# Optimization experiments

Measured on AMD Instinct MI355X. Metric: run time of the kernel, lower is better.

Reference implementation:

```python
import jax, jax.numpy as jnp
import numpy as np

VOCAB = 32000
D = 256          # d_model == hidden_size
L = 2            # num_layers
B, S = 16, 512


def ste_quant_int4(w):
    """Int4 fake-quant with straight-through estimator.
    scale = max|w|/7 (clamped), q = round(w/scale).clip(-8,7)*scale;
    gradient passes through unchanged (identity)."""
    scale = jnp.maximum(jnp.max(jnp.abs(w)) / 7.0, 1e-8)
    q = jnp.round(w / scale).clip(-8.0, 7.0) * scale
    return w + jax.lax.stop_gradient(q - w)


def setup_inputs() -> dict:
    key = jax.random.key(0)
    ks = jax.random.split(key, 8)
    x = jax.random.randint(ks[0], (B, S), 0, VOCAB, dtype=jnp.int32)
    emb_w = jax.random.normal(ks[1], (VOCAB, D), dtype=jnp.float32) * 0.02
    # kaiming-uniform-ish init for linear weights
    lim_ih = 1.0 / np.sqrt(D)
    w_ih = jax.random.uniform(ks[2], (L, 4 * D, D), jnp.float32, -lim_ih, lim_ih)
    w_hh = jax.random.uniform(ks[3], (L, 4 * D, D), jnp.float32, -lim_ih, lim_ih)
    b_ih = jnp.zeros((L, 4 * D), jnp.float32)
    b_hh = jnp.zeros((L, 4 * D), jnp.float32)
    lim_fc = 1.0 / np.sqrt(D)
    fc_w = jax.random.uniform(ks[4], (VOCAB, D), jnp.float32, -lim_fc, lim_fc)
    fc_b = jnp.zeros((VOCAB,), jnp.float32)
    return {"x": x, "emb_w": emb_w, "w_ih": w_ih, "b_ih": b_ih,
            "w_hh": w_hh, "b_hh": b_hh, "fc_w": fc_w, "fc_b": fc_b}


def reference(x, emb_w, w_ih, b_ih, w_hh, b_hh, fc_w, fc_b):
    # quantize each weight once (per-tensor scale, per layer for stacked weights)
    emb_q = ste_quant_int4(emb_w)
    wih_q = jax.vmap(ste_quant_int4)(w_ih)   # [L, 4D, D]
    whh_q = jax.vmap(ste_quant_int4)(w_hh)   # [L, 4D, D]
    fcw_q = ste_quant_int4(fc_w)

    emb = emb_q[x]                            # [B, S, D]
    nlayers = w_ih.shape[0]
    h0 = jnp.zeros((nlayers, x.shape[0], D), emb.dtype)
    c0 = jnp.zeros_like(h0)

    def step(carry, xt):                      # xt: [B, D]
        hs, cs = carry
        h = xt
        new_h, new_c = [], []
        for l in range(nlayers):
            gates = (h @ wih_q[l].T + b_ih[l]
                     + hs[l] @ whh_q[l].T + b_hh[l])   # [B, 4D]
            i, f, g, o = jnp.split(gates, 4, axis=-1)
            i = jax.nn.sigmoid(i)
            f = jax.nn.sigmoid(f)
            g = jnp.tanh(g)
            o = jax.nn.sigmoid(o)
            c = f * cs[l] + i * g
            h = o * jnp.tanh(c)
            new_h.append(h)
            new_c.append(c)
        return (jnp.stack(new_h), jnp.stack(new_c)), h

    (_, _), outs = jax.lax.scan(step, (h0, c0), emb.transpose(1, 0, 2))
    out = outs.transpose(1, 0, 2)             # [B, S, D]
    logits = out @ fcw_q.T + fc_b             # [B, S, VOCAB]
    return logits
```

## Files before the change

### kernel.cpp

```cpp
#include <hip/hip_runtime.h>
#include <hip/hip_bf16.h>
#include <stdint.h>

typedef __attribute__((ext_vector_type(8))) short bf16x8;
typedef __attribute__((ext_vector_type(4))) float f32x4;

#define NB   16
#define SEQ  512
#define DM   256
#define G4   1024
#define VOC  32000
#define TOK  (NB*SEQ)

#define OF_SC     0
#define OF_AMAX   64
#define OF_FLAG   128
#define OF_KEMB   16384
#define OF_KWIH0  (OF_KEMB  + TOK*DM*2)
#define OF_KFC    (OF_KWIH0 + G4*DM*2)
#define OF_WL0    (OF_KFC   + VOC*DM*2)
#define OF_WFF    (OF_WL0   + 512*64*16)
#define OF_WL1    (OF_WFF   + 512*64*16)
#define OF_HX0    (OF_WL1   + 512*64*16)
#define OF_HX1    (OF_HX0   + 4*16384)
#define OF_XG     (OF_HX1   + 4*16384)
#define OF_HOUT   (OF_XG    + (size_t)TOK*G4*4)

__device__ __forceinline__ unsigned short bf16b(float f) {
  __hip_bfloat16 h = __float2bfloat16(f);
  return *reinterpret_cast<unsigned short*>(&h);
}
__device__ __forceinline__ float bf16f(short u) {
  return __uint_as_float(((unsigned)(unsigned short)u) << 16);
}
__device__ __forceinline__ float quant_k_val(float w, float s) {
  float k = rintf(w / s);
  return fminf(fmaxf(k, -8.f), 7.f);
}
__device__ __forceinline__ float sigf(float x) { return 1.f / (1.f + expf(-x)); }

__device__ __forceinline__ void gload_lds16(const void* g, void* l) {
  __builtin_amdgcn_global_load_lds(
      (const __attribute__((address_space(1))) void*)g,
      (__attribute__((address_space(3))) void*)l, 16, 0, 0);
}

__device__ __forceinline__ bf16x8 ld_frag_sys(const void* p) {
  bf16x8 r;
  asm volatile("global_load_dwordx4 %0, %1, off sc0 sc1" : "=v"(r) : "v"(p));
  return r;
}
__device__ __forceinline__ void st_frag_sys(void* p, bf16x8 v) {
  asm volatile("global_store_dwordx4 %0, %1, off sc0 sc1" :: "v"(p), "v"(v) : "memory");
}
__device__ __forceinline__ void vm_drain() {
  asm volatile("s_waitcnt vmcnt(0)" ::: "memory");
  __builtin_amdgcn_sched_barrier(0);
}

__device__ __forceinline__ void spin_ge(int* p, int tgt) {
  int it = 0;
  while (__hip_atomic_load(p, __ATOMIC_RELAXED, __HIP_MEMORY_SCOPE_AGENT) < tgt) {
    __builtin_amdgcn_s_sleep(1);
    if (++it > (1 << 15)) break;
  }
}
__device__ __forceinline__ void flag_set(int* p, int v) {
  __hip_atomic_store(p, v, __ATOMIC_RELAXED, __HIP_MEMORY_SCOPE_AGENT);
}

__global__ void k_init(unsigned int* amax, int* flags) {
  if (threadIdx.x < 8) amax[threadIdx.x] = 0u;
  flags[threadIdx.x] = 0;
}

__global__ void k_absmax(const float* __restrict__ p, int n, unsigned int* amax) {
  float m = 0.f;
  for (int i = blockIdx.x * blockDim.x + threadIdx.x; i < n; i += gridDim.x * blockDim.x)
    m = fmaxf(m, fabsf(p[i]));
  #pragma unroll
  for (int off = 32; off > 0; off >>= 1)
    m = fmaxf(m, __shfl_down(m, off));
  if ((threadIdx.x & 63) == 0) atomicMax(amax, __float_as_uint(m));
}

__global__ void k_finalize(const unsigned int* __restrict__ amax, float* __restrict__ sc) {
  int i = threadIdx.x;
  if (i < 6)       sc[i] = fmaxf(__uint_as_float(amax[i]) / 7.0f, 1e-8f);
  else if (i == 6) sc[i] = 1.0f;
}

__global__ void k_quant_kbf16(const float* __restrict__ src, ushort* __restrict__ dst,
                              int n4, const float* __restrict__ sc, int slot) {
  int i = blockIdx.x * blockDim.x + threadIdx.x;
  if (i >= n4) return;
  const float s = sc[slot];
  float4 w = ((const float4*)src)[i];
  ushort4 o;
  o.x = bf16b(quant_k_val(w.x, s));
  o.y = bf16b(quant_k_val(w.y, s));
  o.z = bf16b(quant_k_val(w.z, s));
  o.w = bf16b(quant_k_val(w.w, s));
  ((ushort4*)dst)[i] = o;
}

__global__ void k_gather(const int* __restrict__ x, const float* __restrict__ emb,
                         const float* __restrict__ sc, ushort* __restrict__ out) {
  int i = blockIdx.x * blockDim.x + threadIdx.x;
  if (i >= TOK * 64) return;
  int tok = i >> 6, d4 = i & 63;
  const float s = sc[0];
  int row = x[tok];
  float4 w = *(const float4*)(emb + (size_t)row * DM + d4 * 4);
  ushort4 o;
  o.x = bf16b(quant_k_val(w.x, s));
  o.y = bf16b(quant_k_val(w.y, s));
  o.z = bf16b(quant_k_val(w.z, s));
  o.w = bf16b(quant_k_val(w.w, s));
  ((ushort4*)out)[i] = o;
}

__global__ void k_packrec(const float* __restrict__ src, bf16x8* __restrict__ dst,
                          const float* __restrict__ sc, int slot, int mode) {
  int q = blockIdx.x * blockDim.x + threadIdx.x;
  if (q >= 512 * 64) return;
  int l = q & 63, kf = (q >> 6) & 7, i = (q >> 9) & 1, w = (q >> 10) & 3, g = (q >> 12) & 7;
  int row = mode ? (g * 128 + (w * 2 + i) * 16 + (l & 15))
                 : (w * 256 + g * 32 + i * 16 + (l & 15));
  int kb = kf * 32 + ((l >> 4) & 3) * 8;
  const float s = sc[slot];
  const float* p = src + (size_t)row * DM + kb;
  bf16x8 o;
  #pragma unroll
  for (int e = 0; e < 8; ++e) o[e] = (short)bf16b(quant_k_val(p[e], s));
  dst[q] = o;
}

__global__ __launch_bounds__(256) void k_gemm(
    const ushort* __restrict__ A, const ushort* __restrict__ B,
    float* __restrict__ C, int M, int N,
    const float* __restrict__ s1, const float* __restrict__ s2,
    const float* __restrict__ bias1, const float* __restrict__ bias2)
{
  __shared__ alignas(16) ushort As[128 * 64];
  __shared__ alignas(16) ushort Bs[128 * 64];
  const int tid  = threadIdx.x;
  const int lane = tid & 63;
  const int wid  = tid >> 6;
  const size_t m0 = (size_t)blockIdx.x * 128;
  const size_t n0 = (size_t)blockIdx.y * 128;
  const int wm = (wid >> 1) * 64;
  const int wn = (wid & 1) * 64;
  const int r  = tid >> 3;
  const int c8 = (tid & 7) * 8;

  f32x4 acc[4][4];
  #pragma unroll
  for (int m = 0; m < 4; ++m)
    #pragma unroll
    for (int n = 0; n < 4; ++n) acc[m][n] = (f32x4){0.f, 0.f, 0.f, 0.f};

  for (int k0 = 0; k0 < DM; k0 += 64) {
    #pragma unroll
    for (int i = 0; i < 4; ++i) {
      gload_lds16(A + (m0 + i * 32 + r) * DM + k0 + c8, (char*)As + i * 4096 + wid * 1024);
      gload_lds16(B + (n0 + i * 32 + r) * DM + k0 + c8, (char*)Bs + i * 4096 + wid * 1024);
    }
    __syncthreads();
    #pragma unroll
    for (int kk = 0; kk < 2; ++kk) {
      const int ko = (kk * 32 + ((lane >> 4) << 3)) * 2;
      bf16x8 af[4], bfr[4];
      #pragma unroll
      for (int m = 0; m < 4; ++m)
        af[m] = *(const bf16x8*)((const char*)As + (wm + m * 16 + (lane & 15)) * 128 + ko);
      #pragma unroll
      for (int n = 0; n < 4; ++n)
        bfr[n] = *(const bf16x8*)((const char*)Bs + (wn + n * 16 + (lane & 15)) * 128 + ko);
      #pragma unroll
      for (int m = 0; m < 4; ++m)
        #pragma unroll
        for (int n = 0; n < 4; ++n)
          acc[m][n] = __builtin_amdgcn_mfma_f32_16x16x32_bf16(af[m], bfr[n], acc[m][n], 0, 0, 0);
    }
    __syncthreads();
  }

  const float alpha = s1[0] * s2[0];
  const int cl = lane & 15;
  const int rq = (lane >> 4) * 4;
  #pragma unroll
  for (int n = 0; n < 4; ++n) {
    const size_t col = n0 + wn + n * 16 + cl;
    float badd = 0.f;
    if (bias1) badd += bias1[col];
    if (bias2) badd += bias2[col];
    #pragma unroll
    for (int m = 0; m < 4; ++m) {
      const size_t rowb = m0 + wm + m * 16 + rq;
      #pragma unroll
      for (int q = 0; q < 4; ++q)
        C[(rowb + q) * (size_t)N + col] = acc[m][n][q] * alpha + badd;
    }
  }
}

__global__ __launch_bounds__(512) void k_rec4(
    const bf16x8* __restrict__ WL0, const bf16x8* __restrict__ WFF,
    const bf16x8* __restrict__ WL1, const float* __restrict__ XG,
    ushort* __restrict__ HX0, ushort* __restrict__ HX1,
    ushort* __restrict__ HOUT, int* __restrict__ flags,
    const float* __restrict__ sc,
    const float* __restrict__ bih, const float* __restrict__ bhh)
{
  if (blockIdx.x & 7) return;
  const int m = blockIdx.x >> 3;
  if (m >= 16) return;
  const int role = m >> 3, g = m & 7;
  const int tid = threadIdx.x, lane = tid & 63, w = tid >> 6;
  const int kg = lane >> 4, cb = lane & 15;
  const int r0 = tid & 31, b = tid >> 5;
  const int gw = (g * 4 + (w >> 1)) * 2 + (w & 1);
  __shared__ float Gl[4 * 32 * 17];
  __shared__ alignas(16) ushort hp[1024];
  int* F0 = flags;
  int* F1 = flags + 8 * 32;
  const int fl = ((r0 >> 3) << 4) | b;

  if (role == 0) {
    bf16x8 a[8];
    #pragma unroll
    for (int c = 0; c < 8; ++c) a[c] = WL0[((gw * 8 + c) << 6) + lane];
    const float s2 = sc[2];
    float cc = 0.f;
    for (int t = 0; t < SEQ; ++t) {
      const size_t xb = ((size_t)(b * 512 + t) << 10) + g * 32 + r0;
      float xv0 = XG[xb], xv1 = XG[xb + 256], xv2 = XG[xb + 512], xv3 = XG[xb + 768];
      if (tid < 16) spin_ge((tid < 8) ? F0 + tid * 32 : F1 + (tid - 8) * 32,
                            (tid < 8) ? t : t - 3);
      __syncthreads();
      f32x4 acc = {0.f, 0.f, 0.f, 0.f};
      if (t > 0) {
        const char* hb = (const char*)HX0 + (size_t)((t - 1) & 3) * 16384 + lane * 16;
        bf16x8 bp[16];
        #pragma unroll
        for (int c = 0; c < 8; ++c) {
          bp[2 * c]     = ld_frag_sys(hb + c * 2048);
          bp[2 * c + 1] = ld_frag_sys(hb + c * 2048 + 1024);
        }
        vm_drain();
        #pragma unroll
        for (int c = 0; c < 8; ++c) {
          acc = __builtin_amdgcn_mfma_f32_16x16x32_bf16(a[c], bp[2 * c],     acc, 0, 0, 0);
          acc = __builtin_amdgcn_mfma_f32_16x16x32_bf16(a[c], bp[2 * c + 1], acc, 0, 0, 0);
        }
      }
      #pragma unroll
      for (int q = 0; q < 4; ++q)
        Gl[((w >> 1) * 32 + (w & 1) * 16 + kg * 4 + q) * 17 + cb] = acc[q];
      __syncthreads();
      {
        float g0 = xv0 + s2 * Gl[(0 * 32 + r0) * 17 + b];
        float g1 = xv1 + s2 * Gl[(1 * 32 + r0) * 17 + b];
        float g2 = xv2 + s2 * Gl[(2 * 32 + r0) * 17 + b];
        float g3 = xv3 + s2 * Gl[(3 * 32 + r0) * 17 + b];
        float i_ = sigf(g0), f_ = sigf(g1), gg = tanhf(g2), o_ = sigf(g3);
        cc = f_ * cc + i_ * gg;
        float h = o_ * tanhf(cc);
        unsigned short p1 = bf16b(h);
        float r1 = h - bf16f((short)p1);
        unsigned short p2 = bf16b(r1);
        hp[fl * 8 + (r0 & 7)]       = p1;
        hp[512 + fl * 8 + (r0 & 7)] = p2;
      }
      __syncthreads();
      if (tid < 128)
        st_frag_sys(HX0 + (size_t)(t & 3) * 8192 + g * 1024 + tid * 8,
                    *(const bf16x8*)(hp + tid * 8));
      vm_drain();
      __syncthreads();
      if (tid == 0) flag_set(F0 + g * 32, t + 1);
    }
  } else {
    bf16x8 aI[8], aH[8];
    #pragma unroll
    for (int c = 0; c < 8; ++c) {
      aI[c] = WFF[((gw * 8 + c) << 6) + lane];
      aH[c] = WL1[((gw * 8 + c) << 6) + lane];
    }
    const float s3 = sc[3], s4 = sc[4];
    const int jb = G4 + g * 32 + r0;
    const float bb0 = bih[jb]       + bhh[jb];
    const float bb1 = bih[jb + 256] + bhh[jb + 256];
    const float bb2 = bih[jb + 512] + bhh[jb + 512];
    const float bb3 = bih[jb + 768] + bhh[jb + 768];
    float cc = 0.f;
    for (int t = 0; t < SEQ; ++t) {
      if (tid < 8) spin_ge(F1 + tid * 32, t);
      __syncthreads();
      f32x4 accH = {0.f, 0.f, 0.f, 0.f};
      if (t > 0) {
        const char* hb = (const char*)HX1 + (size_t)((t - 1) & 3) * 16384 + lane * 16;
        bf16x8 bp[16];
        #pragma unroll
        for (int c = 0; c < 8; ++c) {
          bp[2 * c]     = ld_frag_sys(hb + c * 2048);
          bp[2 * c + 1] = ld_frag_sys(hb + c * 2048 + 1024);
        }
        vm_drain();
        #pragma unroll
        for (int c = 0; c < 8; ++c) {
          accH = __builtin_amdgcn_mfma_f32_16x16x32_bf16(aH[c], bp[2 * c],     accH, 0, 0, 0);
          accH = __builtin_amdgcn_mfma_f32_16x16x32_bf16(aH[c], bp[2 * c + 1], accH, 0, 0, 0);
        }
      }
      if (tid < 8) spin_ge(F0 + tid * 32, t + 1);
      __syncthreads();
      f32x4 accI = {0.f, 0.f, 0.f, 0.f};
      {
        const char* hb = (const char*)HX0 + (size_t)(t & 3) * 16384 + lane * 16;
        bf16x8 bp[16];
        #pragma unroll
        for (int c = 0; c < 8; ++c) {
          bp[2 * c]     = ld_frag_sys(hb + c * 2048);
          bp[2 * c + 1] = ld_frag_sys(hb + c * 2048 + 1024);
        }
        vm_drain();
        #pragma unroll
        for (int c = 0; c < 8; ++c) {
          accI = __builtin_amdgcn_mfma_f32_16x16x32_bf16(aI[c], bp[2 * c],     accI, 0, 0, 0);
          accI = __builtin_amdgcn_mfma_f32_16x16x32_bf16(aI[c], bp[2 * c + 1], accI, 0, 0, 0);
        }
      }
      #pragma unroll
      for (int q = 0; q < 4; ++q)
        Gl[((w >> 1) * 32 + (w & 1) * 16 + kg * 4 + q) * 17 + cb] = s3 * accI[q] + s4 * accH[q];
      __syncthreads();
      {
        float g0 = bb0 + Gl[(0 * 32 + r0) * 17 + b];
        float g1 = bb1 + Gl[(1 * 32 + r0) * 17 + b];
        float g2 = bb2 + Gl[(2 * 32 + r0) * 17 + b];
        float g3 = bb3 + Gl[(3 * 32 + r0) * 17 + b];
        float i_ = sigf(g0), f_ = sigf(g1), gg = tanhf(g2), o_ = sigf(g3);
        cc = f_ * cc + i_ * gg;
        float h = o_ * tanhf(cc);
        unsigned short p1 = bf16b(h);
        float r1 = h - bf16f((short)p1);
        unsigned short p2 = bf16b(r1);
        HOUT[((size_t)b * 512 + t) * 256 + g * 32 + r0] = p1;
        hp[fl * 8 + (r0 & 7)]       = p1;
        hp[512 + fl * 8 + (r0 & 7)] = p2;
      }
      __syncthreads();
      if (tid < 128)
        st_frag_sys(HX1 + (size_t)(t & 3) * 8192 + g * 1024 + tid * 8,
                    *(const bf16x8*)(hp + tid * 8));
      vm_drain();
      __syncthreads();
      if (tid == 0) flag_set(F1 + g * 32, t + 1);
    }
  }
}

extern "C" void kernel_launch(void* const* d_in, const int* in_sizes, int n_in,
                              void* d_out, int out_size, void* d_ws, size_t ws_size,
                              hipStream_t stream) {
  const int*   x   = (const int*)d_in[0];
  const float* emb = (const float*)d_in[1];
  const float* wih = (const float*)d_in[2];
  const float* bih = (const float*)d_in[3];
  const float* whh = (const float*)d_in[4];
  const float* bhh = (const float*)d_in[5];
  const float* fcw = (const float*)d_in[6];
  const float* fcb = (const float*)d_in[7];
  float* out = (float*)d_out;

  char* ws = (char*)d_ws;
  float*        SC    = (float*)(ws + OF_SC);
  unsigned int* AMAX  = (unsigned int*)(ws + OF_AMAX);
  int*          FLAGS = (int*)(ws + OF_FLAG);
  ushort*       KEMB  = (ushort*)(ws + OF_KEMB);
  ushort*       KWIH0 = (ushort*)(ws + OF_KWIH0);
  ushort*       KFC   = (ushort*)(ws + OF_KFC);
  bf16x8*       WL0   = (bf16x8*)(ws + OF_WL0);
  bf16x8*       WFF   = (bf16x8*)(ws + OF_WFF);
  bf16x8*       WL1   = (bf16x8*)(ws + OF_WL1);
  ushort*       HX0   = (ushort*)(ws + OF_HX0);
  ushort*       HX1   = (ushort*)(ws + OF_HX1);
  float*        XG    = (float*)(ws + OF_XG);
  ushort*       HOUT  = (ushort*)(ws + OF_HOUT);

  const int nw = G4 * DM;

  k_init<<<1, 1024, 0, stream>>>(AMAX, FLAGS);
  k_absmax<<<2048, 256, 0, stream>>>(emb,      VOC * DM, AMAX + 0);
  k_absmax<<<256,  256, 0, stream>>>(wih,      nw,       AMAX + 1);
  k_absmax<<<256,  256, 0, stream>>>(whh,      nw,       AMAX + 2);
  k_absmax<<<256,  256, 0, stream>>>(wih + nw, nw,       AMAX + 3);
  k_absmax<<<256,  256, 0, stream>>>(whh + nw, nw,       AMAX + 4);
  k_absmax<<<2048, 256, 0, stream>>>(fcw,      VOC * DM, AMAX + 5);
  k_finalize<<<1, 8, 0, stream>>>(AMAX, SC);

  k_gather<<<TOK * 64 / 256, 256, 0, stream>>>(x, emb, SC, KEMB);
  k_quant_kbf16<<<nw / 4 / 256,       256, 0, stream>>>(wih, KWIH0, nw / 4,       SC, 1);
  k_quant_kbf16<<<VOC * DM / 4 / 256, 256, 0, stream>>>(fcw, KFC,   VOC * DM / 4, SC, 5);
  k_packrec<<<128, 256, 0, stream>>>(whh,      WL0, SC, 2, 0);
  k_packrec<<<128, 256, 0, stream>>>(wih + nw, WFF, SC, 3, 0);
  k_packrec<<<128, 256, 0, stream>>>(whh + nw, WL1, SC, 4, 0);

  dim3 g1(TOK / 128, G4 / 128);
  k_gemm<<<g1, 256, 0, stream>>>(KEMB, KWIH0, XG, TOK, G4, SC + 0, SC + 1, bih, bhh);

  k_rec4<<<128, 512, 0, stream>>>(WL0, WFF, WL1, XG, HX0, HX1, HOUT,
                                  FLAGS, SC, bih, bhh);

  dim3 g2(TOK / 128, VOC / 128);
  k_gemm<<<g2, 256, 0, stream>>>(HOUT, KFC, out, TOK, VOC, SC + 5, SC + 6, fcb, nullptr);
}
```

Before: 2.784 ms.

## Use per-step hidden-state buffers to drop backpressure waits and batch layer-1 loads

Measured after the change: 2.714 ms. 1.03x faster.

```diff
diff --git a/kernel.cpp b/kernel.cpp
--- a/kernel.cpp
+++ b/kernel.cpp
@@ -22,8 +22,8 @@
 #define OF_WFF    (OF_WL0   + 512*64*16)
 #define OF_WL1    (OF_WFF   + 512*64*16)
 #define OF_HX0    (OF_WL1   + 512*64*16)
-#define OF_HX1    (OF_HX0   + 4*16384)
-#define OF_XG     (OF_HX1   + 4*16384)
+#define OF_HX1    (OF_HX0   + (size_t)SEQ*16384)
+#define OF_XG     (OF_HX1   + (size_t)SEQ*16384)
 #define OF_HOUT   (OF_XG    + (size_t)TOK*G4*4)
 
 __device__ __forceinline__ unsigned short bf16b(float f) {
@@ -45,9 +45,9 @@
       (__attribute__((address_space(3))) void*)l, 16, 0, 0);
 }
 
-__device__ __forceinline__ bf16x8 ld_frag_sys(const void* p) {
+__device__ __forceinline__ bf16x8 ld_frag_c(const void* p) {
   bf16x8 r;
-  asm volatile("global_load_dwordx4 %0, %1, off sc0 sc1" : "=v"(r) : "v"(p));
+  asm volatile("global_load_dwordx4 %0, %1, off sc0" : "=v"(r) : "v"(p));
   return r;
 }
 __device__ __forceinline__ void st_frag_sys(void* p, bf16x8 v) {
@@ -55,6 +55,10 @@
 }
 __device__ __forceinline__ void vm_drain() {
   asm volatile("s_waitcnt vmcnt(0)" ::: "memory");
+  __builtin_amdgcn_sched_barrier(0);
+}
+__device__ __forceinline__ void vm_wait16() {
+  asm volatile("s_waitcnt vmcnt(16)" ::: "memory");
   __builtin_amdgcn_sched_barrier(0);
 }
 
@@ -205,7 +209,7 @@
   }
 }
 
-__global__ __launch_bounds__(512) void k_rec4(
+__global__ __launch_bounds__(512) void k_rec5(
     const bf16x8* __restrict__ WL0, const bf16x8* __restrict__ WFF,
     const bf16x8* __restrict__ WL1, const float* __restrict__ XG,
     ushort* __restrict__ HX0, ushort* __restrict__ HX1,
@@ -236,17 +240,16 @@
     for (int t = 0; t < SEQ; ++t) {
       const size_t xb = ((size_t)(b * 512 + t) << 10) + g * 32 + r0;
       float xv0 = XG[xb], xv1 = XG[xb + 256], xv2 = XG[xb + 512], xv3 = XG[xb + 768];
-      if (tid < 16) spin_ge((tid < 8) ? F0 + tid * 32 : F1 + (tid - 8) * 32,
-                            (tid < 8) ? t : t - 3);
+      if (tid < 8) spin_ge(F0 + tid * 32, t);
       __syncthreads();
       f32x4 acc = {0.f, 0.f, 0.f, 0.f};
       if (t > 0) {
-        const char* hb = (const char*)HX0 + (size_t)((t - 1) & 3) * 16384 + lane * 16;
+        const char* hb = (const char*)HX0 + (size_t)(t - 1) * 16384 + lane * 16;
         bf16x8 bp[16];
         #pragma unroll
         for (int c = 0; c < 8; ++c) {
-          bp[2 * c]     = ld_frag_sys(hb + c * 2048);
-          bp[2 * c + 1] = ld_frag_sys(hb + c * 2048 + 1024);
+          bp[2 * c]     = ld_frag_c(hb + c * 2048);
+          bp[2 * c + 1] = ld_frag_c(hb + c * 2048 + 1024);
         }
         vm_drain();
         #pragma unroll
@@ -275,7 +278,7 @@
       }
       __syncthreads();
       if (tid < 128)
-        st_frag_sys(HX0 + (size_t)(t & 3) * 8192 + g * 1024 + tid * 8,
+        st_frag_sys(HX0 + (size_t)t * 8192 + g * 1024 + tid * 8,
                     *(const bf16x8*)(hp + tid * 8));
       vm_drain();
       __syncthreads();
@@ -296,42 +299,37 @@
     const float bb3 = bih[jb + 768] + bhh[jb + 768];
     float cc = 0.f;
     for (int t = 0; t < SEQ; ++t) {
-      if (tid < 8) spin_ge(F1 + tid * 32, t);
-      __syncthreads();
-      f32x4 accH = {0.f, 0.f, 0.f, 0.f};
+      if (tid < 16) spin_ge((tid < 8) ? F1 + tid * 32 : F0 + (tid - 8) * 32,
+                            (tid < 8) ? t : t + 1);
+      __syncthreads();
+      bf16x8 bpH[16], bpI[16];
       if (t > 0) {
-        const char* hb = (const char*)HX1 + (size_t)((t - 1) & 3) * 16384 + lane * 16;
-        bf16x8 bp[16];
+        const char* hb1 = (const char*)HX1 + (size_t)(t - 1) * 16384 + lane * 16;
         #pragma unroll
         for (int c = 0; c < 8; ++c) {
-          bp[2 * c]     = ld_frag_sys(hb + c * 2048);
-          bp[2 * c + 1] = ld_frag_sys(hb + c * 2048 + 1024);
+          bpH[2 * c]     = ld_frag_c(hb1 + c * 2048);
+          bpH[2 * c + 1] = ld_frag_c(hb1 + c * 2048 + 1024);
         }
-        vm_drain();
+      }
+      {
+        const char* hb0 = (const char*)HX0 + (size_t)t * 16384 + lane * 16;
         #pragma unroll
         for (int c = 0; c < 8; ++c) {
-          accH = __builtin_amdgcn_mfma_f32_16x16x32_bf16(aH[c], bp[2 * c],     accH, 0, 0, 0);
-          accH = __builtin_amdgcn_mfma_f32_16x16x32_bf16(aH[c], bp[2 * c + 1], accH, 0, 0, 0);
+          bpI[2 * c]     = ld_frag_c(hb0 + c * 2048);
+          bpI[2 * c + 1] = ld_frag_c(hb0 + c * 2048 + 1024);
         }
       }
-      if (tid < 8) spin_ge(F0 + tid * 32, t + 1);
-      __syncthreads();
-      f32x4 accI = {0.f, 0.f, 0.f, 0.f};
-      {
-        const char* hb = (const char*)HX0 + (size_t)(t & 3) * 16384 + lane * 16;
-        bf16x8 bp[16];
-        #pragma unroll
-        for (int c = 0; c < 8; ++c) {
-          bp[2 * c]     = ld_frag_sys(hb + c * 2048);
-          bp[2 * c + 1] = ld_frag_sys(hb + c * 2048 + 1024);
-        }
-        vm_drain();
-        #pragma unroll
-        for (int c = 0; c < 8; ++c) {
-          accI = __builtin_amdgcn_mfma_f32_16x16x32_bf16(aI[c], bp[2 * c],     accI, 0, 0, 0);
-          accI = __builtin_amdgcn_mfma_f32_16x16x32_bf16(aI[c], bp[2 * c + 1], accI, 0, 0, 0);
-        }
-      }
+      f32x4 accH = {0.f, 0.f, 0.f, 0.f}, accI = {0.f, 0.f, 0.f, 0.f};
+      if (t > 0) {
+        vm_wait16();
+        #pragma unroll
+        for (int c = 0; c < 16; ++c)
+          accH = __builtin_amdgcn_mfma_f32_16x16x32_bf16(aH[c >> 1], bpH[c], accH, 0, 0, 0);
+      }
+      vm_drain();
+      #pragma unroll
+      for (int c = 0; c < 16; ++c)
+        accI = __builtin_amdgcn_mfma_f32_16x16x32_bf16(aI[c >> 1], bpI[c], accI, 0, 0, 0);
       #pragma unroll
       for (int q = 0; q < 4; ++q)
         Gl[((w >> 1) * 32 + (w & 1) * 16 + kg * 4 + q) * 17 + cb] = s3 * accI[q] + s4 * accH[q];
@@ -353,7 +351,7 @@
       }
       __syncthreads();
       if (tid < 128)
-        st_frag_sys(HX1 + (size_t)(t & 3) * 8192 + g * 1024 + tid * 8,
+        st_frag_sys(HX1 + (size_t)t * 8192 + g * 1024 + tid * 8,
                     *(const bf16x8*)(hp + tid * 8));
       vm_drain();
       __syncthreads();
@@ -411,7 +409,7 @@
   dim3 g1(TOK / 128, G4 / 128);
   k_gemm<<<g1, 256, 0, stream>>>(KEMB, KWIH0, XG, TOK, G4, SC + 0, SC + 1, bih, bhh);
 
-  k_rec4<<<128, 512, 0, stream>>>(WL0, WFF, WL1, XG, HX0, HX1, HOUT,
+  k_rec5<<<128, 512, 0, stream>>>(WL0, WFF, WL1, XG, HX0, HX1, HOUT,
                                   FLAGS, SC, bih, bhh);
 
   dim3 g2(TOK / 128, VOC / 128);
```
